# Kernel tuning notes

Hardware: AMD Instinct MI355X
Metric: run time of the kernel (lower is better)

## Reference

```python
import jax, jax.numpy as jnp
import numpy as np

N = 2048
IN_C, HID, LAT = 128, 128, 64
E_SPARSE = 65536


def gcn_conv(x, W, b, src, dst, w, n):
    # PyG GCNConv: h = D^-1/2 (A+I) D^-1/2 (x W) + b  (self-loops already in edge list)
    deg = jax.ops.segment_sum(w, dst, num_segments=n)
    dinv = jnp.where(deg > 0, jax.lax.rsqrt(deg), 0.0)
    norm = dinv[src] * w * dinv[dst]            # [E]
    h = x @ W                                   # [N, out]
    agg = jax.ops.segment_sum(h[src] * norm[:, None], dst, num_segments=n)
    return agg + b


def setup_inputs() -> dict:
    key = jax.random.key(0)
    ks = jax.random.split(key, 9)
    x = jax.random.normal(ks[0], (N, IN_C), jnp.float32)
    masked_y = jax.random.normal(ks[1], (N, N), jnp.float32)
    edge_index = jax.random.randint(ks[2], (2, E_SPARSE), 0, N, dtype=jnp.int32)
    s = 0.05
    W1 = jax.random.normal(ks[3], (IN_C, HID), jnp.float32) * s
    b1 = jnp.zeros((HID,), jnp.float32)
    Wmu = jax.random.normal(ks[4], (HID, LAT), jnp.float32) * s
    bmu = jnp.zeros((LAT,), jnp.float32)
    Wls = jax.random.normal(ks[5], (HID, LAT), jnp.float32) * s
    bls = jnp.zeros((LAT,), jnp.float32)
    return {"x": x, "masked_y": masked_y, "W1": W1, "b1": b1,
            "Wmu": Wmu, "bmu": bmu, "Wls": Wls, "bls": bls,
            "edge_index": edge_index}


def reference(x, masked_y, W1, b1, Wmu, bmu, Wls, bls, edge_index):
    n = x.shape[0]
    half = n // 2
    # masking leaves only the top-left [half, half] block of masked_y nonzero;
    # dense_to_sparse on that block -> all half*half (row, col) pairs (entries != 0 a.s.)
    rows = jnp.repeat(jnp.arange(half, dtype=edge_index.dtype), half)
    cols = jnp.tile(jnp.arange(half, dtype=edge_index.dtype), half)
    y_w = jax.nn.sigmoid(masked_y[:half, :half].reshape(-1))
    loop = jnp.arange(n, dtype=edge_index.dtype)
    src = jnp.concatenate([edge_index[0], rows, loop])
    dst = jnp.concatenate([edge_index[1], cols, loop])
    w = jnp.concatenate([jnp.ones((edge_index.shape[1],), x.dtype), y_w,
                         jnp.ones((n,), x.dtype)])
    hidden = jax.nn.relu(gcn_conv(x, W1, b1, src, dst, w, n))
    z_mu = gcn_conv(hidden, Wmu, bmu, src, dst, w, n)
    z_logstd = gcn_conv(hidden, Wls, bls, src, dst, w, n)
    return (z_mu, z_logstd)
```

## Files before the change

### kernel.cpp

```cpp
#include <hip/hip_runtime.h>

#define NN 2048
#define HALF 1024
#define CC 128
#define EE 65536
#define CAP 128

typedef unsigned short u16;

__device__ __forceinline__ float sigm(float v){ return 1.0f/(1.0f + __expf(-v)); }

__device__ __forceinline__ float dinv_lo(int i, const int* __restrict__ cnt,
                                         const float* __restrict__ colsum){
  return rsqrtf(1.0f + (float)cnt[i] + colsum[i]);
}
__device__ __forceinline__ float dinv_any(int i, const int* __restrict__ cnt,
                                          const float* __restrict__ colsum){
  float cs = (i < HALF) ? colsum[i] : 0.0f;
  return rsqrtf(1.0f + (float)cnt[i] + cs);
}

__global__ __launch_bounds__(256) void k_prep(
    const float* __restrict__ my, const int* __restrict__ ei, const float* __restrict__ x,
    const float* __restrict__ W1,
    const float* __restrict__ bmu, const float* __restrict__ bls,
    float* __restrict__ SpRaw, float* __restrict__ colsum,
    int* __restrict__ cnt, u16* __restrict__ bucket, float* __restrict__ H0,
    float* __restrict__ AGG1, float* __restrict__ out)
{
  __shared__ float la[8][CC];
  int b = blockIdx.x, t = threadIdx.x;
  int gid = b*256 + t;
  if (gid < 65536) {
    ((float4*)AGG1)[gid] = make_float4(0.f,0.f,0.f,0.f);
  } else if (gid < 131072) {
    int i = gid - 65536;
    int g4 = (i & 15)*4;
    const float* bb = (i < 32768) ? bmu : bls;
    ((float4*)out)[i] = make_float4(bb[g4], bb[g4+1], bb[g4+2], bb[g4+3]);
  }

  if (b < 128) {
    int c0 = t*4;
    float cs0=0.f, cs1=0.f, cs2=0.f, cs3=0.f;
    #pragma unroll 2
    for (int rr=0; rr<8; ++rr){
      int r = b*8 + rr;
      float4 v = *(const float4*)(my + (size_t)r*NN + c0);
      float s0=sigm(v.x), s1=sigm(v.y), s2=sigm(v.z), s3=sigm(v.w);
      *(float4*)(SpRaw + (size_t)r*HALF + c0) = make_float4(s0,s1,s2,s3);
      cs0+=s0; cs1+=s1; cs2+=s2; cs3+=s3;
    }
    atomicAdd(&colsum[c0+0], cs0);
    atomicAdd(&colsum[c0+1], cs1);
    atomicAdd(&colsum[c0+2], cs2);
    atomicAdd(&colsum[c0+3], cs3);
  } else if (b < 384) {
    int e = (b-128)*256 + t;
    int s = ei[e], d = ei[EE + e];
    int slot = atomicAdd(&cnt[d], 1);
    if (slot < CAP) bucket[d*CAP + slot] = (u16)s;
  } else {
    int row0 = (b-384)*8;
    #pragma unroll
    for (int i=0;i<4;i++){
      int idx = i*256 + t;
      la[idx>>7][idx&127] = x[(size_t)row0*CC + idx];
    }
    __syncthreads();
    int f = t & 127, rh = t >> 7;
    float o[4] = {0.f,0.f,0.f,0.f};
    #pragma unroll 4
    for (int k=0;k<CC;k++){
      float w = W1[k*CC + f];
      o[0] = fmaf(la[rh*4+0][k], w, o[0]);
      o[1] = fmaf(la[rh*4+1][k], w, o[1]);
      o[2] = fmaf(la[rh*4+2][k], w, o[2]);
      o[3] = fmaf(la[rh*4+3][k], w, o[3]);
    }
    #pragma unroll
    for (int i=0;i<4;i++)
      H0[(size_t)(row0 + rh*4 + i)*CC + f] = o[i];
  }
}

__global__ __launch_bounds__(256) void k_layer1(
  const float* __restrict__ SpRaw, const float* __restrict__ F,
  const int* __restrict__ cnt, const float* __restrict__ colsum,
  const u16* __restrict__ bucket, float* __restrict__ AGG)
{
  __shared__ float ld[256];
  int b = blockIdx.x, t = threadIdx.x;
  if (b < 256) {
    int f = t & 127, half = t >> 7;
    int dbase = (b>>2)*16 + half*8;
    int r0 = (b&3)*256;
    ld[t] = dinv_lo(r0 + t, cnt, colsum);
    __syncthreads();
    float acc[8];
    #pragma unroll
    for (int j=0;j<8;j++) acc[j] = 0.f;
    #pragma unroll 4
    for (int rr=0; rr<256; ++rr){
      int r = r0 + rr;
      float fv = F[(size_t)r*CC + f] * ld[rr];
      const float4* sp4 = (const float4*)(SpRaw + (size_t)r*HALF + dbase);
      float4 s0 = sp4[0], s1 = sp4[1];
      acc[0] = fmaf(s0.x, fv, acc[0]);
      acc[1] = fmaf(s0.y, fv, acc[1]);
      acc[2] = fmaf(s0.z, fv, acc[2]);
      acc[3] = fmaf(s0.w, fv, acc[3]);
      acc[4] = fmaf(s1.x, fv, acc[4]);
      acc[5] = fmaf(s1.y, fv, acc[5]);
      acc[6] = fmaf(s1.z, fv, acc[6]);
      acc[7] = fmaf(s1.w, fv, acc[7]);
    }
    #pragma unroll
    for (int j=0;j<8;j++)
      atomicAdd(&AGG[(size_t)(dbase+j)*CC + f], acc[j]*dinv_lo(dbase+j, cnt, colsum));
  } else {
    int idx = b - 256;
    int d = idx*2 + (t>>7), f = t & 127;
    float dd = dinv_any(d, cnt, colsum);
    float acc = dd * F[(size_t)d*CC + f];
    int m = cnt[d]; m = m > CAP ? CAP : m;
    const u16* bk = bucket + d*CAP;
    for (int j=0;j<m;j++){
      int s = bk[j];
      acc = fmaf(dinv_any(s, cnt, colsum), F[(size_t)s*CC + f], acc);
    }
    atomicAdd(&AGG[(size_t)d*CC + f], dd*acc);
  }
}

__global__ __launch_bounds__(256) void k_mid(
  const float* __restrict__ AGG1, const float* __restrict__ b1,
  const float* __restrict__ Wmu, const float* __restrict__ Wls,
  const int* __restrict__ cnt, const float* __restrict__ colsum,
  float* __restrict__ G)
{
  __shared__ float la[8][CC];
  int b = blockIdx.x, t = threadIdx.x;
  int row0 = b*8;
  #pragma unroll
  for (int i=0;i<4;i++){
    int idx = i*256 + t;
    float v = AGG1[(size_t)row0*CC + idx] + b1[idx & 127];
    la[idx>>7][idx&127] = v > 0.f ? v : 0.f;
  }
  __syncthreads();
  int f = t & 127, rh = t >> 7;
  int g = f & 63;
  const float* W = (f < 64) ? Wmu : Wls;
  float o[4] = {0.f,0.f,0.f,0.f};
  #pragma unroll 4
  for (int k=0;k<CC;k++){
    float w = W[k*64 + g];
    o[0] = fmaf(la[rh*4+0][k], w, o[0]);
    o[1] = fmaf(la[rh*4+1][k], w, o[1]);
    o[2] = fmaf(la[rh*4+2][k], w, o[2]);
    o[3] = fmaf(la[rh*4+3][k], w, o[3]);
  }
  #pragma unroll
  for (int i=0;i<4;i++){
    int row = row0 + rh*4 + i;
    G[(size_t)row*CC + f] = o[i] * dinv_any(row, cnt, colsum);
  }
}

__global__ __launch_bounds__(256) void k_layer2(
  const float* __restrict__ SpRaw, const float* __restrict__ G,
  const int* __restrict__ cnt, const float* __restrict__ colsum,
  const u16* __restrict__ bucket, float* __restrict__ out)
{
  int b = blockIdx.x, t = threadIdx.x;
  int f = t & 127, g = f & 63;
  size_t obase = (f < 64) ? 0 : (size_t)NN*64;
  if (b < 256) {
    int half = t >> 7;
    int dbase = (b>>2)*16 + half*8;
    int r0 = (b&3)*256;
    float acc[8];
    #pragma unroll
    for (int j=0;j<8;j++) acc[j] = 0.f;
    #pragma unroll 4
    for (int r=r0; r<r0+256; ++r){
      float fv = G[(size_t)r*CC + f];
      const float4* sp4 = (const float4*)(SpRaw + (size_t)r*HALF + dbase);
      float4 s0 = sp4[0], s1 = sp4[1];
      acc[0] = fmaf(s0.x, fv, acc[0]);
      acc[1] = fmaf(s0.y, fv, acc[1]);
      acc[2] = fmaf(s0.z, fv, acc[2]);
      acc[3] = fmaf(s0.w, fv, acc[3]);
      acc[4] = fmaf(s1.x, fv, acc[4]);
      acc[5] = fmaf(s1.y, fv, acc[5]);
      acc[6] = fmaf(s1.z, fv, acc[6]);
      acc[7] = fmaf(s1.w, fv, acc[7]);
    }
    #pragma unroll
    for (int j=0;j<8;j++)
      atomicAdd(&out[obase + (size_t)(dbase+j)*64 + g],
                acc[j]*dinv_lo(dbase+j, cnt, colsum));
  } else {
    int idx = b - 256;
    int d = idx*2 + (t>>7);
    float acc = G[(size_t)d*CC + f];
    int m = cnt[d]; m = m > CAP ? CAP : m;
    const u16* bk = bucket + d*CAP;
    for (int j=0;j<m;j++){
      int s = bk[j];
      acc += G[(size_t)s*CC + f];
    }
    atomicAdd(&out[obase + (size_t)d*64 + g], acc * dinv_any(d, cnt, colsum));
  }
}

extern "C" void kernel_launch(void* const* d_in, const int* in_sizes, int n_in,
                              void* d_out, int out_size, void* d_ws, size_t ws_size,
                              hipStream_t stream)
{
  (void)in_sizes; (void)n_in; (void)out_size; (void)ws_size;
  const float* x   = (const float*)d_in[0];
  const float* my  = (const float*)d_in[1];
  const float* W1  = (const float*)d_in[2];
  const float* b1  = (const float*)d_in[3];
  const float* Wmu = (const float*)d_in[4];
  const float* bmu = (const float*)d_in[5];
  const float* Wls = (const float*)d_in[6];
  const float* bls = (const float*)d_in[7];
  const int*   ei  = (const int*)d_in[8];
  float* out = (float*)d_out;
  char* ws = (char*)d_ws;

  int*   cnt    = (int*)  (ws + 0);
  float* colsum = (float*)(ws + 8192);
  float* AGG1   = (float*)(ws + 12288);
  u16*   bucket = (u16*)  (ws + 1060864);
  float* SpRaw  = (float*)(ws + 1585152);
  float* H0     = (float*)(ws + 5779456);
  float* G      = (float*)(ws + 6828032);

  hipMemsetAsync(ws, 0, 12288, stream);
  k_prep  <<<640,  256, 0, stream>>>(my, ei, x, W1, bmu, bls,
                                     SpRaw, colsum, cnt, bucket, H0, AGG1, out);
  k_layer1<<<1280, 256, 0, stream>>>(SpRaw, H0, cnt, colsum, bucket, AGG1);
  k_mid   <<<256,  256, 0, stream>>>(AGG1, b1, Wmu, Wls, cnt, colsum, G);
  k_layer2<<<1280, 256, 0, stream>>>(SpRaw, G, cnt, colsum, bucket, out);
}
```

Measured before the change: 173.9 us.

## Remap layer kernels to 2 features x 4 dests per thread, cache dinv in LDS

Both aggregation kernels now give each thread 2 features and 4 destinations instead of 1 feature and 8 destinations. Each wave reads one float4 of SpRaw per row instead of two, and the sparse gather blocks handle 4 nodes each, which cuts the grid from 1280 to 768 blocks. Layer 1 precomputes all dinv values into shared memory in every block, so per-edge rsqrt and global lookups go away, at the cost of a 2048-entry prologue per block. The small GEMMs read LDS as float4, and the sparse loops load index pairs two at a time.

```diff
diff --git a/kernel.cpp b/kernel.cpp
--- a/kernel.cpp
+++ b/kernel.cpp
@@ -69,18 +69,27 @@
     }
     __syncthreads();
     int f = t & 127, rh = t >> 7;
-    float o[4] = {0.f,0.f,0.f,0.f};
+    const float4* a0 = (const float4*)la[rh*4+0];
+    const float4* a1 = (const float4*)la[rh*4+1];
+    const float4* a2 = (const float4*)la[rh*4+2];
+    const float4* a3 = (const float4*)la[rh*4+3];
+    float o0=0.f, o1=0.f, o2=0.f, o3=0.f;
     #pragma unroll 4
-    for (int k=0;k<CC;k++){
-      float w = W1[k*CC + f];
-      o[0] = fmaf(la[rh*4+0][k], w, o[0]);
-      o[1] = fmaf(la[rh*4+1][k], w, o[1]);
-      o[2] = fmaf(la[rh*4+2][k], w, o[2]);
-      o[3] = fmaf(la[rh*4+3][k], w, o[3]);
-    }
-    #pragma unroll
-    for (int i=0;i<4;i++)
-      H0[(size_t)(row0 + rh*4 + i)*CC + f] = o[i];
+    for (int k4=0;k4<32;k4++){
+      float4 v0=a0[k4], v1=a1[k4], v2=a2[k4], v3=a3[k4];
+      float w0 = W1[(k4*4+0)*CC + f];
+      float w1 = W1[(k4*4+1)*CC + f];
+      float w2 = W1[(k4*4+2)*CC + f];
+      float w3 = W1[(k4*4+3)*CC + f];
+      o0=fmaf(v0.x,w0,o0); o0=fmaf(v0.y,w1,o0); o0=fmaf(v0.z,w2,o0); o0=fmaf(v0.w,w3,o0);
+      o1=fmaf(v1.x,w0,o1); o1=fmaf(v1.y,w1,o1); o1=fmaf(v1.z,w2,o1); o1=fmaf(v1.w,w3,o1);
+      o2=fmaf(v2.x,w0,o2); o2=fmaf(v2.y,w1,o2); o2=fmaf(v2.z,w2,o2); o2=fmaf(v2.w,w3,o2);
+      o3=fmaf(v3.x,w0,o3); o3=fmaf(v3.y,w1,o3); o3=fmaf(v3.z,w2,o3); o3=fmaf(v3.w,w3,o3);
+    }
+    H0[(size_t)(row0 + rh*4 + 0)*CC + f] = o0;
+    H0[(size_t)(row0 + rh*4 + 1)*CC + f] = o1;
+    H0[(size_t)(row0 + rh*4 + 2)*CC + f] = o2;
+    H0[(size_t)(row0 + rh*4 + 3)*CC + f] = o3;
   }
 }
 
@@ -89,47 +98,63 @@
   const int* __restrict__ cnt, const float* __restrict__ colsum,
   const u16* __restrict__ bucket, float* __restrict__ AGG)
 {
-  __shared__ float ld[256];
-  int b = blockIdx.x, t = threadIdx.x;
+  __shared__ float sdinv[NN];
+  int b = blockIdx.x, t = threadIdx.x;
+  #pragma unroll
+  for (int i=0;i<8;i++){
+    int j = i*256 + t;
+    float cs = (j < HALF) ? colsum[j] : 0.0f;
+    sdinv[j] = rsqrtf(1.0f + (float)cnt[j] + cs);
+  }
+  __syncthreads();
+  int lane = t & 63, f0 = lane*2;
   if (b < 256) {
-    int f = t & 127, half = t >> 7;
-    int dbase = (b>>2)*16 + half*8;
+    int dbase = (b>>2)*16 + (t>>6)*4;
     int r0 = (b&3)*256;
-    ld[t] = dinv_lo(r0 + t, cnt, colsum);
-    __syncthreads();
-    float acc[8];
-    #pragma unroll
-    for (int j=0;j<8;j++) acc[j] = 0.f;
+    float a00=0.f,a01=0.f,a10=0.f,a11=0.f,a20=0.f,a21=0.f,a30=0.f,a31=0.f;
     #pragma unroll 4
     for (int rr=0; rr<256; ++rr){
       int r = r0 + rr;
-      float fv = F[(size_t)r*CC + f] * ld[rr];
-      const float4* sp4 = (const float4*)(SpRaw + (size_t)r*HALF + dbase);
-      float4 s0 = sp4[0], s1 = sp4[1];
-      acc[0] = fmaf(s0.x, fv, acc[0]);
-      acc[1] = fmaf(s0.y, fv, acc[1]);
-      acc[2] = fmaf(s0.z, fv, acc[2]);
-      acc[3] = fmaf(s0.w, fv, acc[3]);
-      acc[4] = fmaf(s1.x, fv, acc[4]);
-      acc[5] = fmaf(s1.y, fv, acc[5]);
-      acc[6] = fmaf(s1.z, fv, acc[6]);
-      acc[7] = fmaf(s1.w, fv, acc[7]);
-    }
-    #pragma unroll
-    for (int j=0;j<8;j++)
-      atomicAdd(&AGG[(size_t)(dbase+j)*CC + f], acc[j]*dinv_lo(dbase+j, cnt, colsum));
+      float2 fv = *(const float2*)(F + (size_t)r*CC + f0);
+      float sc = sdinv[r];
+      float fx = fv.x*sc, fy = fv.y*sc;
+      float4 s4 = *(const float4*)(SpRaw + (size_t)r*HALF + dbase);
+      a00=fmaf(s4.x,fx,a00); a01=fmaf(s4.x,fy,a01);
+      a10=fmaf(s4.y,fx,a10); a11=fmaf(s4.y,fy,a11);
+      a20=fmaf(s4.z,fx,a20); a21=fmaf(s4.z,fy,a21);
+      a30=fmaf(s4.w,fx,a30); a31=fmaf(s4.w,fy,a31);
+    }
+    float d0=sdinv[dbase+0], d1=sdinv[dbase+1], d2=sdinv[dbase+2], d3=sdinv[dbase+3];
+    float* o = AGG + (size_t)dbase*CC + f0;
+    atomicAdd(o + 0*CC + 0, a00*d0); atomicAdd(o + 0*CC + 1, a01*d0);
+    atomicAdd(o + 1*CC + 0, a10*d1); atomicAdd(o + 1*CC + 1, a11*d1);
+    atomicAdd(o + 2*CC + 0, a20*d2); atomicAdd(o + 2*CC + 1, a21*d2);
+    atomicAdd(o + 3*CC + 0, a30*d3); atomicAdd(o + 3*CC + 1, a31*d3);
   } else {
-    int idx = b - 256;
-    int d = idx*2 + (t>>7), f = t & 127;
-    float dd = dinv_any(d, cnt, colsum);
-    float acc = dd * F[(size_t)d*CC + f];
+    int d = (b-256)*4 + (t>>6);
+    float dd = sdinv[d];
+    float2 sv = *(const float2*)(F + (size_t)d*CC + f0);
+    float ax = dd*sv.x, ay = dd*sv.y;
     int m = cnt[d]; m = m > CAP ? CAP : m;
     const u16* bk = bucket + d*CAP;
-    for (int j=0;j<m;j++){
-      int s = bk[j];
-      acc = fmaf(dinv_any(s, cnt, colsum), F[(size_t)s*CC + f], acc);
-    }
-    atomicAdd(&AGG[(size_t)d*CC + f], dd*acc);
+    int j = 0;
+    for (; j+1 < m; j += 2){
+      unsigned pr = *(const unsigned*)(bk + j);
+      int s0 = pr & 0xffff, s1 = pr >> 16;
+      float w0 = sdinv[s0], w1 = sdinv[s1];
+      float2 v0 = *(const float2*)(F + (size_t)s0*CC + f0);
+      float2 v1 = *(const float2*)(F + (size_t)s1*CC + f0);
+      ax = fmaf(w0, v0.x, ax); ay = fmaf(w0, v0.y, ay);
+      ax = fmaf(w1, v1.x, ax); ay = fmaf(w1, v1.y, ay);
+    }
+    if (j < m){
+      int s0 = bk[j];
+      float w0 = sdinv[s0];
+      float2 v0 = *(const float2*)(F + (size_t)s0*CC + f0);
+      ax = fmaf(w0, v0.x, ax); ay = fmaf(w0, v0.y, ay);
+    }
+    atomicAdd(&AGG[(size_t)d*CC + f0    ], dd*ax);
+    atomicAdd(&AGG[(size_t)d*CC + f0 + 1], dd*ay);
   }
 }
 
@@ -152,20 +177,29 @@
   int f = t & 127, rh = t >> 7;
   int g = f & 63;
   const float* W = (f < 64) ? Wmu : Wls;
-  float o[4] = {0.f,0.f,0.f,0.f};
+  const float4* a0 = (const float4*)la[rh*4+0];
+  const float4* a1 = (const float4*)la[rh*4+1];
+  const float4* a2 = (const float4*)la[rh*4+2];
+  const float4* a3 = (const float4*)la[rh*4+3];
+  float o0=0.f, o1=0.f, o2=0.f, o3=0.f;
   #pragma unroll 4
-  for (int k=0;k<CC;k++){
-    float w = W[k*64 + g];
-    o[0] = fmaf(la[rh*4+0][k], w, o[0]);
-    o[1] = fmaf(la[rh*4+1][k], w, o[1]);
-    o[2] = fmaf(la[rh*4+2][k], w, o[2]);
-    o[3] = fmaf(la[rh*4+3][k], w, o[3]);
-  }
-  #pragma unroll
-  for (int i=0;i<4;i++){
-    int row = row0 + rh*4 + i;
-    G[(size_t)row*CC + f] = o[i] * dinv_any(row, cnt, colsum);
-  }
+  for (int k4=0;k4<32;k4++){
+    float4 v0=a0[k4], v1=a1[k4], v2=a2[k4], v3=a3[k4];
+    float w0 = W[(k4*4+0)*64 + g];
+    float w1 = W[(k4*4+1)*64 + g];
+    float w2 = W[(k4*4+2)*64 + g];
+    float w3 = W[(k4*4+3)*64 + g];
+    o0=fmaf(v0.x,w0,o0); o0=fmaf(v0.y,w1,o0); o0=fmaf(v0.z,w2,o0); o0=fmaf(v0.w,w3,o0);
+    o1=fmaf(v1.x,w0,o1); o1=fmaf(v1.y,w1,o1); o1=fmaf(v1.z,w2,o1); o1=fmaf(v1.w,w3,o1);
+    o2=fmaf(v2.x,w0,o2); o2=fmaf(v2.y,w1,o2); o2=fmaf(v2.z,w2,o2); o2=fmaf(v2.w,w3,o2);
+    o3=fmaf(v3.x,w0,o3); o3=fmaf(v3.y,w1,o3); o3=fmaf(v3.z,w2,o3); o3=fmaf(v3.w,w3,o3);
+  }
+  {
+    int row = row0 + rh*4 + 0; G[(size_t)row*CC + f] = o0 * dinv_any(row, cnt, colsum);
+  }
+  { int row = row0 + rh*4 + 1; G[(size_t)row*CC + f] = o1 * dinv_any(row, cnt, colsum); }
+  { int row = row0 + rh*4 + 2; G[(size_t)row*CC + f] = o2 * dinv_any(row, cnt, colsum); }
+  { int row = row0 + rh*4 + 3; G[(size_t)row*CC + f] = o3 * dinv_any(row, cnt, colsum); }
 }
 
 __global__ __launch_bounds__(256) void k_layer2(
@@ -174,44 +208,52 @@
   const u16* __restrict__ bucket, float* __restrict__ out)
 {
   int b = blockIdx.x, t = threadIdx.x;
-  int f = t & 127, g = f & 63;
-  size_t obase = (f < 64) ? 0 : (size_t)NN*64;
+  int lane = t & 63, f0 = lane*2;
+  size_t obase = (f0 < 64) ? 0 : (size_t)NN*64;
+  int g0 = f0 & 63;
   if (b < 256) {
-    int half = t >> 7;
-    int dbase = (b>>2)*16 + half*8;
+    int dbase = (b>>2)*16 + (t>>6)*4;
     int r0 = (b&3)*256;
-    float acc[8];
-    #pragma unroll
-    for (int j=0;j<8;j++) acc[j] = 0.f;
+    float a00=0.f,a01=0.f,a10=0.f,a11=0.f,a20=0.f,a21=0.f,a30=0.f,a31=0.f;
     #pragma unroll 4
-    for (int r=r0; r<r0+256; ++r){
-      float fv = G[(size_t)r*CC + f];
-      const float4* sp4 = (const float4*)(SpRaw + (size_t)r*HALF + dbase);
-      float4 s0 = sp4[0], s1 = sp4[1];
-      acc[0] = fmaf(s0.x, fv, acc[0]);
-      acc[1] = fmaf(s0.y, fv, acc[1]);
-      acc[2] = fmaf(s0.z, fv, acc[2]);
-      acc[3] = fmaf(s0.w, fv, acc[3]);
-      acc[4] = fmaf(s1.x, fv, acc[4]);
-      acc[5] = fmaf(s1.y, fv, acc[5]);
-      acc[6] = fmaf(s1.z, fv, acc[6]);
-      acc[7] = fmaf(s1.w, fv, acc[7]);
-    }
-    #pragma unroll
-    for (int j=0;j<8;j++)
-      atomicAdd(&out[obase + (size_t)(dbase+j)*64 + g],
-                acc[j]*dinv_lo(dbase+j, cnt, colsum));
+    for (int rr=0; rr<256; ++rr){
+      int r = r0 + rr;
+      float2 gv = *(const float2*)(G + (size_t)r*CC + f0);
+      float4 s4 = *(const float4*)(SpRaw + (size_t)r*HALF + dbase);
+      a00=fmaf(s4.x,gv.x,a00); a01=fmaf(s4.x,gv.y,a01);
+      a10=fmaf(s4.y,gv.x,a10); a11=fmaf(s4.y,gv.y,a11);
+      a20=fmaf(s4.z,gv.x,a20); a21=fmaf(s4.z,gv.y,a21);
+      a30=fmaf(s4.w,gv.x,a30); a31=fmaf(s4.w,gv.y,a31);
+    }
+    float d0=dinv_lo(dbase+0,cnt,colsum), d1=dinv_lo(dbase+1,cnt,colsum);
+    float d2=dinv_lo(dbase+2,cnt,colsum), d3=dinv_lo(dbase+3,cnt,colsum);
+    float* o = out + obase + (size_t)dbase*64 + g0;
+    atomicAdd(o + 0*64 + 0, a00*d0); atomicAdd(o + 0*64 + 1, a01*d0);
+    atomicAdd(o + 1*64 + 0, a10*d1); atomicAdd(o + 1*64 + 1, a11*d1);
+    atomicAdd(o + 2*64 + 0, a20*d2); atomicAdd(o + 2*64 + 1, a21*d2);
+    atomicAdd(o + 3*64 + 0, a30*d3); atomicAdd(o + 3*64 + 1, a31*d3);
   } else {
-    int idx = b - 256;
-    int d = idx*2 + (t>>7);
-    float acc = G[(size_t)d*CC + f];
+    int d = (b-256)*4 + (t>>6);
+    float2 a = *(const float2*)(G + (size_t)d*CC + f0);
+    float ax = a.x, ay = a.y;
     int m = cnt[d]; m = m > CAP ? CAP : m;
     const u16* bk = bucket + d*CAP;
-    for (int j=0;j<m;j++){
-      int s = bk[j];
-      acc += G[(size_t)s*CC + f];
-    }
-    atomicAdd(&out[obase + (size_t)d*64 + g], acc * dinv_any(d, cnt, colsum));
+    int j = 0;
+    for (; j+1 < m; j += 2){
+      unsigned pr = *(const unsigned*)(bk + j);
+      int s0 = pr & 0xffff, s1 = pr >> 16;
+      float2 v0 = *(const float2*)(G + (size_t)s0*CC + f0);
+      float2 v1 = *(const float2*)(G + (size_t)s1*CC + f0);
+      ax += v0.x + v1.x; ay += v0.y + v1.y;
+    }
+    if (j < m){
+      int s0 = bk[j];
+      float2 v0 = *(const float2*)(G + (size_t)s0*CC + f0);
+      ax += v0.x; ay += v0.y;
+    }
+    float dd = dinv_any(d, cnt, colsum);
+    atomicAdd(&out[obase + (size_t)d*64 + g0    ], dd*ax);
+    atomicAdd(&out[obase + (size_t)d*64 + g0 + 1], dd*ay);
   }
 }
 
@@ -241,9 +283,9 @@
   float* G      = (float*)(ws + 6828032);
 
   hipMemsetAsync(ws, 0, 12288, stream);
-  k_prep  <<<640,  256, 0, stream>>>(my, ei, x, W1, bmu, bls,
-                                     SpRaw, colsum, cnt, bucket, H0, AGG1, out);
-  k_layer1<<<1280, 256, 0, stream>>>(SpRaw, H0, cnt, colsum, bucket, AGG1);
-  k_mid   <<<256,  256, 0, stream>>>(AGG1, b1, Wmu, Wls, cnt, colsum, G);
-  k_layer2<<<1280, 256, 0, stream>>>(SpRaw, G, cnt, colsum, bucket, out);
-}
+  k_prep  <<<640, 256, 0, stream>>>(my, ei, x, W1, bmu, bls,
+                                    SpRaw, colsum, cnt, bucket, H0, AGG1, out);
+  k_layer1<<<768, 256, 0, stream>>>(SpRaw, H0, cnt, colsum, bucket, AGG1);
+  k_mid   <<<256, 256, 0, stream>>>(AGG1, b1, Wmu, Wls, cnt, colsum, G);
+  k_layer2<<<768, 256, 0, stream>>>(SpRaw, G, cnt, colsum, bucket, out);
+}
```

Result: faster. 162.0 us (-6.8%).
